# Optimization experiments

Hardware: AMD Instinct MI355X
Metric: run time of the kernel (lower is better)

The kernel has to match this reference:

```python
import jax, jax.numpy as jnp
import numpy as np

N_NODES = 50000
N_EDGES = 1600000
N_HEAD = 4
F_OUT = 128


def setup_inputs() -> dict:
    key = jax.random.key(0)
    k1, k2, k3, k4 = jax.random.split(key, 4)
    x = jax.random.normal(k1, (N_NODES, F_OUT), dtype=jnp.float32)
    # diag weight [H,1,F]; small scale like xavier on a diag-ish param
    w = jax.random.normal(k2, (N_HEAD, 1, F_OUT), dtype=jnp.float32) * 0.1
    # a_src_dst init: uniform(-stdv, stdv), stdv = 1/sqrt(2*f_out)
    stdv = 1.0 / np.sqrt(2 * F_OUT)
    a = jax.random.uniform(k3, (N_HEAD, 2 * F_OUT, 1), dtype=jnp.float32, minval=-stdv, maxval=stdv)
    edge_index = jax.random.randint(k4, (2, N_EDGES), 0, N_NODES, dtype=jnp.int64)
    return {"x": x, "w": w, "a": a, "edge_index": edge_index}


def reference(x, w, a, edge_index):
    # x: [N,F], w: [H,1,F] (diag), a: [H,2F,1], edge_index: [2,E]
    H, F = w.shape[0], w.shape[-1]
    N = x.shape[0]
    src = edge_index[0]  # row indices (aggregation targets)
    dst = edge_index[1]
    h = x[None, :, :] * w  # [H,N,F]  (diag: elementwise scale per head)
    # split cat(h_src,h_dst)@a into two per-node projections (same math as concat+matmul)
    a_src = a[:, :F, 0]  # [H,F]
    a_dst = a[:, F:, 0]  # [H,F]
    s_src = jnp.einsum('hnf,hf->hn', h, a_src)  # [H,N]
    s_dst = jnp.einsum('hnf,hf->hn', h, a_dst)  # [H,N]
    score = s_src[:, src] + s_dst[:, dst]  # [H,E]
    edge_e = jnp.exp(-jax.nn.leaky_relu(score, negative_slope=0.2))  # [H,E]
    outs = []
    for i in range(H):  # small fixed head loop keeps peak memory at one head's messages
        rowsum = jax.ops.segment_sum(edge_e[i], src, num_segments=N)  # [N]
        msg = edge_e[i][:, None] * h[i][dst]  # [E,F]
        agg = jax.ops.segment_sum(msg, src, num_segments=N)  # [N,F]
        outs.append(agg / rowsum[:, None])
    return jnp.stack(outs, axis=0)  # [H,N,F]
```

## Files before the change

kernel.cpp:

```cpp
#include <hip/hip_runtime.h>

#define N_NODES 50000
#define N_EDGES 1600000
#define N_HEAD 4
#define F_OUT 128
#define CAP 96
#define NPS 512
#define K1 98
#define SCAP 17408
#define NPG 16
#define GROUPS 3125
#define EPB 2048
#define P1_BLOCKS ((N_EDGES + EPB - 1) / EPB)

__global__ void __launch_bounds__(256) score_kernel(
    const float* __restrict__ x, const float* __restrict__ w,
    const float* __restrict__ a, float4* __restrict__ s_src4,
    float4* __restrict__ s_dst4, int* __restrict__ gc) {
  if (blockIdx.x == 0 && threadIdx.x < K1) gc[threadIdx.x] = 0;
  int wv = (blockIdx.x * blockDim.x + threadIdx.x) >> 6;
  int lane = threadIdx.x & 63;
  if (wv >= N_NODES) return;
  float xv0 = x[wv * F_OUT + lane];
  float xv1 = x[wv * F_OUT + 64 + lane];
  float ps[N_HEAD], pd[N_HEAD];
#pragma unroll
  for (int h = 0; h < N_HEAD; ++h) {
    float w0 = w[h * F_OUT + lane];
    float w1 = w[h * F_OUT + 64 + lane];
    float as0 = a[h * 2 * F_OUT + lane];
    float as1 = a[h * 2 * F_OUT + 64 + lane];
    float ad0 = a[h * 2 * F_OUT + F_OUT + lane];
    float ad1 = a[h * 2 * F_OUT + F_OUT + 64 + lane];
    ps[h] = xv0 * w0 * as0 + xv1 * w1 * as1;
    pd[h] = xv0 * w0 * ad0 + xv1 * w1 * ad1;
  }
#pragma unroll
  for (int off = 32; off > 0; off >>= 1) {
#pragma unroll
    for (int h = 0; h < N_HEAD; ++h) {
      ps[h] += __shfl_xor(ps[h], off, 64);
      pd[h] += __shfl_xor(pd[h], off, 64);
    }
  }
  if (lane == 0) {
    s_src4[wv] = make_float4(ps[0], ps[1], ps[2], ps[3]);
    s_dst4[wv] = make_float4(pd[0], pd[1], pd[2], pd[3]);
  }
}

__global__ void __launch_bounds__(256) partition_kernel(
    const int* __restrict__ src, const int* __restrict__ dst,
    int* __restrict__ gc, unsigned int* __restrict__ region) {
  __shared__ int hist[K1], cur[K1], lstart[K1], gpos[K1];
  __shared__ unsigned int staging[EPB];
  const int tid = threadIdx.x;
  const int base = blockIdx.x * EPB;
  int vc = N_EDGES - base;
  if (vc > EPB) vc = EPB;

  unsigned int pk[EPB / 256];
#pragma unroll
  for (int k = 0; k < EPB / 256; ++k) {
    int i = k * 256 + tid;
    if (i < vc) {
      unsigned int s = (unsigned int)src[base + i];
      unsigned int d = (unsigned int)dst[base + i];
      pk[k] = (s << 16) | d;
    } else {
      pk[k] = 0xffffffffu;
    }
  }
  if (tid < K1) { hist[tid] = 0; cur[tid] = 0; }
  __syncthreads();
#pragma unroll
  for (int k = 0; k < EPB / 256; ++k)
    if (pk[k] != 0xffffffffu) atomicAdd(&hist[pk[k] >> 25], 1);
  __syncthreads();
  if (tid < 64) {
    int carry = 0;
    for (int b0 = 0; b0 < K1; b0 += 64) {
      int idx = b0 + tid;
      int h = (idx < K1) ? hist[idx] : 0;
      int v = h;
#pragma unroll
      for (int off = 1; off < 64; off <<= 1) {
        int t = __shfl_up(v, off, 64);
        if (tid >= off) v += t;
      }
      if (idx < K1) {
        lstart[idx] = carry + v - h;
        gpos[idx] = atomicAdd(&gc[idx], h);
      }
      carry += __shfl(v, 63, 64);
    }
  }
  __syncthreads();
#pragma unroll
  for (int k = 0; k < EPB / 256; ++k) {
    if (pk[k] != 0xffffffffu) {
      int b = pk[k] >> 25;
      int pos = lstart[b] + atomicAdd(&cur[b], 1);
      staging[pos] = pk[k];
    }
  }
  __syncthreads();
  for (int i = tid; i < vc; i += 256) {
    unsigned int v = staging[i];
    int b = v >> 25;
    int off = gpos[b] + (i - lstart[b]);
    if (off < SCAP) region[(size_t)b * SCAP + off] = v;
  }
}

__global__ void __launch_bounds__(256, 8) agg_kernel(
    const float* __restrict__ x, const float* __restrict__ w,
    const float4* __restrict__ s_src4, const float4* __restrict__ s_dst4,
    const int* __restrict__ gc, const unsigned int* __restrict__ region,
    float* __restrict__ out) {
  __shared__ int ncnt[NPG];
  __shared__ int nbkt[NPG][CAP];
  __shared__ float4 lds_w[4][CAP];
  const int tid = threadIdx.x;
  const int g = blockIdx.x;
  const int sb = g >> 5;
  int c = gc[sb];
  if (c > SCAP) c = SCAP;
  if (tid < NPG) ncnt[tid] = 0;
  __syncthreads();

  const unsigned int* reg = region + (size_t)sb * SCAP;
  const unsigned int gtag = (unsigned int)g;
  for (int i = tid; i < c; i += 256) {
    unsigned int v = reg[i];
    unsigned int s = v >> 16;
    if ((s >> 4) == gtag) {
      int l = s & 15;
      int p = atomicAdd(&ncnt[l], 1);
      if (p < CAP) nbkt[l][p] = (int)(v & 0xffffu);
    }
  }
  __syncthreads();

  const int ws = tid >> 6, lane = tid & 63;
  const int half = lane >> 5, fl = lane & 31;
  const float4* __restrict__ xq = (const float4*)x;
  const float4* __restrict__ wq = (const float4*)w;

  for (int l = ws; l < NPG; l += 4) {
    int n = g * NPG + l;
    if (n >= N_NODES) break;
    int m = ncnt[l];
    m = (m < CAP) ? m : CAP;
    float4 ss = s_src4[n];

    float p0 = 0.f, p1 = 0.f, p2 = 0.f, p3 = 0.f;
    for (int j = lane; j < m; j += 64) {
      int d = nbkt[l][j];
      float4 sd = s_dst4[d];
      float sc0 = ss.x + sd.x, sc1 = ss.y + sd.y, sc2 = ss.z + sd.z, sc3 = ss.w + sd.w;
      float e0 = __expf(-fmaxf(sc0, 0.2f * sc0));
      float e1 = __expf(-fmaxf(sc1, 0.2f * sc1));
      float e2 = __expf(-fmaxf(sc2, 0.2f * sc2));
      float e3 = __expf(-fmaxf(sc3, 0.2f * sc3));
      lds_w[ws][j] = make_float4(e0, e1, e2, e3);
      p0 += e0; p1 += e1; p2 += e2; p3 += e3;
    }
#pragma unroll
    for (int off = 32; off > 0; off >>= 1) {
      p0 += __shfl_xor(p0, off, 64);
      p1 += __shfl_xor(p1, off, 64);
      p2 += __shfl_xor(p2, off, 64);
      p3 += __shfl_xor(p3, off, 64);
    }

    float4 A0 = {0, 0, 0, 0}, A1 = {0, 0, 0, 0}, A2 = {0, 0, 0, 0}, A3 = {0, 0, 0, 0};
    int j = 0;
    for (; j + 3 < m; j += 4) {
      int da = nbkt[l][j + half];
      int db = nbkt[l][j + 2 + half];
      float4 wa = lds_w[ws][j + half];
      float4 wb = lds_w[ws][j + 2 + half];
      float4 xa = xq[(size_t)da * 32 + fl];
      float4 xb = xq[(size_t)db * 32 + fl];
      A0.x = fmaf(wa.x, xa.x, A0.x); A0.y = fmaf(wa.x, xa.y, A0.y);
      A0.z = fmaf(wa.x, xa.z, A0.z); A0.w = fmaf(wa.x, xa.w, A0.w);
      A1.x = fmaf(wa.y, xa.x, A1.x); A1.y = fmaf(wa.y, xa.y, A1.y);
      A1.z = fmaf(wa.y, xa.z, A1.z); A1.w = fmaf(wa.y, xa.w, A1.w);
      A2.x = fmaf(wa.z, xa.x, A2.x); A2.y = fmaf(wa.z, xa.y, A2.y);
      A2.z = fmaf(wa.z, xa.z, A2.z); A2.w = fmaf(wa.z, xa.w, A2.w);
      A3.x = fmaf(wa.w, xa.x, A3.x); A3.y = fmaf(wa.w, xa.y, A3.y);
      A3.z = fmaf(wa.w, xa.z, A3.z); A3.w = fmaf(wa.w, xa.w, A3.w);
      A0.x = fmaf(wb.x, xb.x, A0.x); A0.y = fmaf(wb.x, xb.y, A0.y);
      A0.z = fmaf(wb.x, xb.z, A0.z); A0.w = fmaf(wb.x, xb.w, A0.w);
      A1.x = fmaf(wb.y, xb.x, A1.x); A1.y = fmaf(wb.y, xb.y, A1.y);
      A1.z = fmaf(wb.y, xb.z, A1.z); A1.w = fmaf(wb.y, xb.w, A1.w);
      A2.x = fmaf(wb.z, xb.x, A2.x); A2.y = fmaf(wb.z, xb.y, A2.y);
      A2.z = fmaf(wb.z, xb.z, A2.z); A2.w = fmaf(wb.z, xb.w, A2.w);
      A3.x = fmaf(wb.w, xb.x, A3.x); A3.y = fmaf(wb.w, xb.y, A3.y);
      A3.z = fmaf(wb.w, xb.z, A3.z); A3.w = fmaf(wb.w, xb.w, A3.w);
    }
    for (; j + 1 < m; j += 2) {
      int da = nbkt[l][j + half];
      float4 wa = lds_w[ws][j + half];
      float4 xa = xq[(size_t)da * 32 + fl];
      A0.x = fmaf(wa.x, xa.x, A0.x); A0.y = fmaf(wa.x, xa.y, A0.y);
      A0.z = fmaf(wa.x, xa.z, A0.z); A0.w = fmaf(wa.x, xa.w, A0.w);
      A1.x = fmaf(wa.y, xa.x, A1.x); A1.y = fmaf(wa.y, xa.y, A1.y);
      A1.z = fmaf(wa.y, xa.z, A1.z); A1.w = fmaf(wa.y, xa.w, A1.w);
      A2.x = fmaf(wa.z, xa.x, A2.x); A2.y = fmaf(wa.z, xa.y, A2.y);
      A2.z = fmaf(wa.z, xa.z, A2.z); A2.w = fmaf(wa.z, xa.w, A2.w);
      A3.x = fmaf(wa.w, xa.x, A3.x); A3.y = fmaf(wa.w, xa.y, A3.y);
      A3.z = fmaf(wa.w, xa.z, A3.z); A3.w = fmaf(wa.w, xa.w, A3.w);
    }
    if (j < m) {
      int da = nbkt[l][j];
      float4 wa = lds_w[ws][j];
      float4 xa = xq[(size_t)da * 32 + fl];
      if (half == 0) {
        A0.x = fmaf(wa.x, xa.x, A0.x); A0.y = fmaf(wa.x, xa.y, A0.y);
        A0.z = fmaf(wa.x, xa.z, A0.z); A0.w = fmaf(wa.x, xa.w, A0.w);
        A1.x = fmaf(wa.y, xa.x, A1.x); A1.y = fmaf(wa.y, xa.y, A1.y);
        A1.z = fmaf(wa.y, xa.z, A1.z); A1.w = fmaf(wa.y, xa.w, A1.w);
        A2.x = fmaf(wa.z, xa.x, A2.x); A2.y = fmaf(wa.z, xa.y, A2.y);
        A2.z = fmaf(wa.z, xa.z, A2.z); A2.w = fmaf(wa.z, xa.w, A2.w);
        A3.x = fmaf(wa.w, xa.x, A3.x); A3.y = fmaf(wa.w, xa.y, A3.y);
        A3.z = fmaf(wa.w, xa.z, A3.z); A3.w = fmaf(wa.w, xa.w, A3.w);
      }
    }

    A0.x += __shfl_xor(A0.x, 32, 64); A0.y += __shfl_xor(A0.y, 32, 64);
    A0.z += __shfl_xor(A0.z, 32, 64); A0.w += __shfl_xor(A0.w, 32, 64);
    A1.x += __shfl_xor(A1.x, 32, 64); A1.y += __shfl_xor(A1.y, 32, 64);
    A1.z += __shfl_xor(A1.z, 32, 64); A1.w += __shfl_xor(A1.w, 32, 64);
    A2.x += __shfl_xor(A2.x, 32, 64); A2.y += __shfl_xor(A2.y, 32, 64);
    A2.z += __shfl_xor(A2.z, 32, 64); A2.w += __shfl_xor(A2.w, 32, 64);
    A3.x += __shfl_xor(A3.x, 32, 64); A3.y += __shfl_xor(A3.y, 32, 64);
    A3.z += __shfl_xor(A3.z, 32, 64); A3.w += __shfl_xor(A3.w, 32, 64);

    float r0 = 1.f / p0, r1 = 1.f / p1, r2 = 1.f / p2, r3 = 1.f / p3;

    {
      float4 acc; float rr; int h;
      if (half == 0) { acc = A0; rr = r0; h = 0; } else { acc = A1; rr = r1; h = 1; }
      float4 ww = wq[h * 32 + fl];
      float4 o = {ww.x * acc.x * rr, ww.y * acc.y * rr,
                  ww.z * acc.z * rr, ww.w * acc.w * rr};
      ((float4*)out)[((size_t)h * N_NODES + n) * 32 + fl] = o;
    }
    {
      float4 acc; float rr; int h;
      if (half == 0) { acc = A2; rr = r2; h = 2; } else { acc = A3; rr = r3; h = 3; }
      float4 ww = wq[h * 32 + fl];
      float4 o = {ww.x * acc.x * rr, ww.y * acc.y * rr,
                  ww.z * acc.z * rr, ww.w * acc.w * rr};
      ((float4*)out)[((size_t)h * N_NODES + n) * 32 + fl] = o;
    }
  }
}

extern "C" void kernel_launch(void* const* d_in, const int* in_sizes, int n_in,
                              void* d_out, int out_size, void* d_ws, size_t ws_size,
                              hipStream_t stream) {
  const float* x = (const float*)d_in[0];
  const float* w = (const float*)d_in[1];
  const float* a = (const float*)d_in[2];
  const int* ei = (const int*)d_in[3];
  const int* src = ei;
  const int* dst = ei + N_EDGES;
  float* out = (float*)d_out;

  char* p = (char*)d_ws;
  float4* s_src4 = (float4*)p;      p += (size_t)N_NODES * 16;
  float4* s_dst4 = (float4*)p;      p += (size_t)N_NODES * 16;
  int* gc = (int*)p;                p += 4096;
  unsigned int* region = (unsigned int*)p;
  p += (size_t)K1 * SCAP * 4;

  score_kernel<<<(N_NODES * 64 + 255) / 256, 256, 0, stream>>>(x, w, a, s_src4, s_dst4, gc);
  partition_kernel<<<P1_BLOCKS, 256, 0, stream>>>(src, dst, gc, region);
  agg_kernel<<<GROUPS, 256, 0, stream>>>(x, w, s_src4, s_dst4, gc, region, out);
}
```

Before: 333.1 us.

## Pre-sort superbucket entries by group so agg blocks read only their own slice

```diff
diff --git a/kernel.cpp b/kernel.cpp
--- a/kernel.cpp
+++ b/kernel.cpp
@@ -10,7 +10,8 @@
 #define SCAP 17408
 #define NPG 16
 #define GROUPS 3125
-#define EPB 2048
+#define GPS 32
+#define EPB 4096
 #define P1_BLOCKS ((N_EDGES + EPB - 1) / EPB)
 
 __global__ void __launch_bounds__(256) score_kernel(
@@ -113,32 +114,64 @@
   }
 }
 
+__global__ void __launch_bounds__(512) group_sort_kernel(
+    const int* __restrict__ gc, unsigned int* __restrict__ region,
+    int* __restrict__ gstart, int* __restrict__ gcnt) {
+  __shared__ unsigned int staging[SCAP];
+  __shared__ int hist[GPS], start[GPS], cur[GPS];
+  const int sb = blockIdx.x;
+  const int tid = threadIdx.x;
+  int c = gc[sb];
+  if (c > SCAP) c = SCAP;
+  unsigned int* reg = region + (size_t)sb * SCAP;
+  if (tid < GPS) { hist[tid] = 0; cur[tid] = 0; }
+  __syncthreads();
+  for (int i = tid; i < c; i += 512)
+    atomicAdd(&hist[(reg[i] >> 20) & (GPS - 1)], 1);
+  __syncthreads();
+  if (tid < GPS) {
+    int h = hist[tid];
+    int v = h;
+#pragma unroll
+    for (int off = 1; off < GPS; off <<= 1) {
+      int t = __shfl_up(v, off, 64);
+      if (tid >= off) v += t;
+    }
+    start[tid] = v - h;
+    gstart[sb * GPS + tid] = sb * SCAP + (v - h);
+    gcnt[sb * GPS + tid] = h;
+  }
+  __syncthreads();
+  for (int i = tid; i < c; i += 512) {
+    unsigned int v = reg[i];
+    int l = (v >> 20) & (GPS - 1);
+    int p = start[l] + atomicAdd(&cur[l], 1);
+    staging[p] = v;
+  }
+  __syncthreads();
+  for (int i = tid; i < c; i += 512) reg[i] = staging[i];
+}
+
 __global__ void __launch_bounds__(256, 8) agg_kernel(
     const float* __restrict__ x, const float* __restrict__ w,
     const float4* __restrict__ s_src4, const float4* __restrict__ s_dst4,
-    const int* __restrict__ gc, const unsigned int* __restrict__ region,
-    float* __restrict__ out) {
+    const unsigned int* __restrict__ region, const int* __restrict__ gstart,
+    const int* __restrict__ gcnt, float* __restrict__ out) {
   __shared__ int ncnt[NPG];
   __shared__ int nbkt[NPG][CAP];
   __shared__ float4 lds_w[4][CAP];
   const int tid = threadIdx.x;
   const int g = blockIdx.x;
-  const int sb = g >> 5;
-  int c = gc[sb];
-  if (c > SCAP) c = SCAP;
   if (tid < NPG) ncnt[tid] = 0;
   __syncthreads();
 
-  const unsigned int* reg = region + (size_t)sb * SCAP;
-  const unsigned int gtag = (unsigned int)g;
-  for (int i = tid; i < c; i += 256) {
-    unsigned int v = reg[i];
-    unsigned int s = v >> 16;
-    if ((s >> 4) == gtag) {
-      int l = s & 15;
-      int p = atomicAdd(&ncnt[l], 1);
-      if (p < CAP) nbkt[l][p] = (int)(v & 0xffffu);
-    }
+  const int s0 = gstart[g];
+  const int cnt = gcnt[g];
+  for (int i = tid; i < cnt; i += 256) {
+    unsigned int v = region[s0 + i];
+    int l = (v >> 16) & (NPG - 1);
+    int p = atomicAdd(&ncnt[l], 1);
+    if (p < CAP) nbkt[l][p] = (int)(v & 0xffffu);
   }
   __syncthreads();
 
@@ -239,7 +272,6 @@
     A3.z += __shfl_xor(A3.z, 32, 64); A3.w += __shfl_xor(A3.w, 32, 64);
 
     float r0 = 1.f / p0, r1 = 1.f / p1, r2 = 1.f / p2, r3 = 1.f / p3;
-
     {
       float4 acc; float rr; int h;
       if (half == 0) { acc = A0; rr = r0; h = 0; } else { acc = A1; rr = r1; h = 1; }
@@ -274,10 +306,13 @@
   float4* s_src4 = (float4*)p;      p += (size_t)N_NODES * 16;
   float4* s_dst4 = (float4*)p;      p += (size_t)N_NODES * 16;
   int* gc = (int*)p;                p += 4096;
+  int* gstart = (int*)p;            p += (size_t)K1 * GPS * 4;
+  int* gcnt = (int*)p;              p += (size_t)K1 * GPS * 4;
   unsigned int* region = (unsigned int*)p;
   p += (size_t)K1 * SCAP * 4;
 
   score_kernel<<<(N_NODES * 64 + 255) / 256, 256, 0, stream>>>(x, w, a, s_src4, s_dst4, gc);
   partition_kernel<<<P1_BLOCKS, 256, 0, stream>>>(src, dst, gc, region);
-  agg_kernel<<<GROUPS, 256, 0, stream>>>(x, w, s_src4, s_dst4, gc, region, out);
-}
+  group_sort_kernel<<<K1, 512, 0, stream>>>(gc, region, gstart, gcnt);
+  agg_kernel<<<GROUPS, 256, 0, stream>>>(x, w, s_src4, s_dst4, region, gstart, gcnt, out);
+}
```

Result: faster. 310.6 us (-6.8%).
